# Kernel optimization log

Hardware: AMD Instinct MI355X
Metric: run time of the kernel (lower is better)

## Reference

```python
import jax, jax.numpy as jnp
import numpy as np

N, BOND, PHYS = 784, 4, 2
BS = 16384
STD = 1e-08


def setup_inputs() -> dict:
    key = jax.random.key(0)
    k1, k2 = jax.random.split(key)
    data = jax.random.randint(k1, (BS, N), 0, 2).astype(jnp.float32)
    bias = jnp.eye(BOND, dtype=jnp.float32)[:, :, None].repeat(PHYS, axis=2)  # (BOND,BOND,PHYS)
    tensors = STD * jax.random.normal(k2, (N, BOND, BOND, PHYS), dtype=jnp.float32) + bias
    return {"data": data, "tensors": tensors}


def reference(data, tensors):
    # data: (bs, n) in {0,1}; tensors: (n, D, D, P)
    bs, n = data.shape
    emb = jnp.stack([data, 1.0 - data], axis=2)  # (bs, n, P)
    # per-site transfer matrices for every sample: (n, bs, D, D)
    mats = jnp.einsum('nlri,bni->nblr', tensors, emb)
    left0 = mats[0][:, 0, :]  # (bs, D)  -- row 0 of site-0 matrix
    lx0 = jax.nn.log_softmax(tensors[0, 0, 0])  # (P,)

    def step(left, xs):
        t, m = xs  # t: (D, D, P), m: (bs, D, D)
        logits = left @ t[:, 0, :]              # (bs, P)
        lx = jax.nn.log_softmax(logits, axis=1)  # (bs, P)
        new_left = jnp.einsum('bl,blr->br', left, m)
        return new_left, lx

    _, lxs = jax.lax.scan(step, left0, (tensors[1:], mats[1:]))  # (n-1, bs, P)
    logx = jnp.concatenate(
        [jnp.broadcast_to(lx0, (1, bs, PHYS)), lxs], axis=0)  # (n, bs, P)
    logx = jnp.transpose(logx, (1, 0, 2))  # (bs, n, P)
    log_prob = logx[..., 0] * data + logx[..., 1] * (1.0 - data)
    return log_prob.sum(-1)  # (bs,)
```

## Files before the change

kernel.cpp:

```cpp
#include <hip/hip_runtime.h>

#define NSITES 784
#define BS_TOT 16384
#define KSEG 16
#define GSEG 49
#define NQUAD 12

typedef unsigned long long u64;

#define STEPV(sbit, TP, L0,L1,L2,L3, AN, AL) do {                                    \
    const float* t_ = (TP);                                                          \
    float p00 = fmaf(L0, t_[0],  fmaf(L1, t_[8],  fmaf(L2, t_[16], L3 * t_[24])));   \
    float p01 = fmaf(L0, t_[1],  fmaf(L1, t_[9],  fmaf(L2, t_[17], L3 * t_[25])));   \
    float p10 = fmaf(L0, t_[2],  fmaf(L1, t_[10], fmaf(L2, t_[18], L3 * t_[26])));   \
    float p11 = fmaf(L0, t_[3],  fmaf(L1, t_[11], fmaf(L2, t_[19], L3 * t_[27])));   \
    float p20 = fmaf(L0, t_[4],  fmaf(L1, t_[12], fmaf(L2, t_[20], L3 * t_[28])));   \
    float p21 = fmaf(L0, t_[5],  fmaf(L1, t_[13], fmaf(L2, t_[21], L3 * t_[29])));   \
    float p30 = fmaf(L0, t_[6],  fmaf(L1, t_[14], fmaf(L2, t_[22], L3 * t_[30])));   \
    float p31 = fmaf(L0, t_[7],  fmaf(L1, t_[15], fmaf(L2, t_[23], L3 * t_[31])));   \
    bool s_ = (sbit);                                                                \
    float mx_ = fmaxf(p00, p01);                                                     \
    float ch_ = s_ ? p00 : p01;                                                      \
    AN += (ch_ - mx_);                                                               \
    float ad_ = fabsf(p00 - p01);                                                    \
    AL += __builtin_amdgcn_logf(1.0f + __builtin_amdgcn_exp2f(-ad_ * 1.4426950408889634f)); \
    L0 = s_ ? p00 : p01;                                                             \
    L1 = s_ ? p10 : p11;                                                             \
    L2 = s_ ? p20 : p21;                                                             \
    L3 = s_ ? p30 : p31;                                                             \
} while (0)

#define STEP(sbit, TP) STEPV(sbit, TP, left0,left1,left2,left3, acc_nat, acc_l2)

#define MM_ROW(Q, Pr) do {                                                           \
    Q.x = fmaf(Pr.x, m0.x, fmaf(Pr.y, m1.x, fmaf(Pr.z, m2.x, Pr.w * m3.x)));         \
    Q.y = fmaf(Pr.x, m0.y, fmaf(Pr.y, m1.y, fmaf(Pr.z, m2.y, Pr.w * m3.y)));         \
    Q.z = fmaf(Pr.x, m0.z, fmaf(Pr.y, m1.z, fmaf(Pr.z, m2.z, Pr.w * m3.z)));         \
    Q.w = fmaf(Pr.x, m0.w, fmaf(Pr.y, m1.w, fmaf(Pr.z, m2.w, Pr.w * m3.w)));         \
} while (0)

#define MM4(P0,P1,P2,P3) do { float4 Q0,Q1,Q2,Q3; \
    MM_ROW(Q0,P0); MM_ROW(Q1,P1); MM_ROW(Q2,P2); MM_ROW(Q3,P3); \
    P0=Q0; P1=Q1; P2=Q2; P3=Q3; } while (0)

__global__ __launch_bounds__(256) void fused_pre_kernel(const float* __restrict__ tensors,
                                                        const float* __restrict__ data,
                                                        float* __restrict__ QQ,
                                                        u64* __restrict__ packed) {
    if (blockIdx.x < KSEG) {
        __shared__ float sPP[24][4][16];
        const int k = blockIdx.x;
        const int t = threadIdx.x;
        const int n0 = k * GSEG;

        if (t < 96) {
            const int j = t >> 2, c2 = t & 3;
            const float* t0 = tensors + (size_t)(n0 + 2 * j) * 32;
            const float* t1 = tensors + (size_t)(n0 + 2 * j + 1) * 32;
            const int p0 = (c2 & 1) ? 0 : 1;
            const int p1 = (c2 & 2) ? 0 : 1;
            float A[4][4], B[4][4];
            #pragma unroll
            for (int l = 0; l < 4; ++l)
                #pragma unroll
                for (int r = 0; r < 4; ++r) {
                    A[l][r] = t0[l * 8 + r * 2 + p0];
                    B[l][r] = t1[l * 8 + r * 2 + p1];
                }
            #pragma unroll
            for (int a = 0; a < 4; ++a)
                #pragma unroll
                for (int bb = 0; bb < 4; ++bb)
                    sPP[j][c2][a * 4 + bb] =
                        fmaf(A[a][0], B[0][bb], fmaf(A[a][1], B[1][bb],
                        fmaf(A[a][2], B[2][bb], A[a][3] * B[3][bb])));
        }
        __syncthreads();

        if (t < 192) {
            const int q = t >> 4, c = t & 15;
            const float* A = sPP[2 * q][c & 3];
            const float* B = sPP[2 * q + 1][(c >> 2) & 3];
            float* dst = QQ + ((size_t)(k * NQUAD + q) * 16 + c) * 16;
            #pragma unroll
            for (int a = 0; a < 4; ++a)
                #pragma unroll
                for (int bb = 0; bb < 4; ++bb)
                    dst[a * 4 + bb] =
                        fmaf(A[a * 4 + 0], B[0 * 4 + bb], fmaf(A[a * 4 + 1], B[1 * 4 + bb],
                        fmaf(A[a * 4 + 2], B[2 * 4 + bb], A[a * 4 + 3] * B[3 * 4 + bb])));
        }
    } else {
        int gid  = (blockIdx.x - KSEG) * 256 + threadIdx.x;
        int row  = gid >> 6;
        int lane = threadIdx.x & 63;
        const float* r = data + (size_t)row * NSITES;
        #pragma unroll
        for (int w = 0; w < 12; ++w) {
            u64 m = __ballot(r[w * 64 + lane] == 1.0f);
            if (lane == 0) packed[(size_t)w * BS_TOT + row] = m;
        }
        float v = (lane < 16) ? r[768 + lane] : 0.0f;
        u64 m = __ballot((lane < 16) && (v == 1.0f));
        if (lane == 0) packed[(size_t)12 * BS_TOT + row] = m;
    }
}

__device__ __forceinline__ u64 bit_window(const u64* __restrict__ packed, int n0, int b) {
    int a0 = n0 >> 6, s = n0 & 63;
    u64 w0 = packed[(size_t)a0 * BS_TOT + b];
    u64 w1 = packed[(size_t)(a0 + 1) * BS_TOT + b];
    return s ? ((w0 >> s) | (w1 << (64 - s))) : w0;
}

__global__ __launch_bounds__(256) void phase1q_kernel(const float* __restrict__ tensors,
                                                      const u64* __restrict__ packed,
                                                      const float* __restrict__ QQ,
                                                      float* __restrict__ Pbuf) {
    const int b = blockIdx.x * 256 + threadIdx.x;
    const int k = blockIdx.y;
    const int n0 = k * GSEG;

    __shared__ __align__(16) float lt[NQUAD * 16 * 20];
    {
        const float4* src = (const float4*)(QQ + (size_t)k * NQUAD * 16 * 16);
        float4* dst = (float4*)lt;
        for (int e = threadIdx.x; e < NQUAD * 16 * 4; e += 256) {
            int q = e >> 6, c = (e >> 2) & 15, j = e & 3;
            dst[q * 80 + c * 5 + j] = src[e];
        }
    }
    __syncthreads();

    u64 win = bit_window(packed, n0, b);
    const float4* ltf4 = (const float4*)lt;

    float4 P0, P1, P2, P3;
    {
        const int c0 = (int)(win & 15ull);
        const float4* mi = ltf4 + (c0 * 5);
        P0 = mi[0]; P1 = mi[1]; P2 = mi[2]; P3 = mi[3];
    }
    #pragma unroll
    for (int q = 1; q < NQUAD; ++q) {
        const int cq = (int)((win >> (4 * q)) & 15ull);
        const float4* mi = ltf4 + (q * 80 + cq * 5);
        float4 m0 = mi[0], m1 = mi[1], m2 = mi[2], m3 = mi[3];
        MM4(P0, P1, P2, P3);
    }
    {
        const float* t48 = tensors + (size_t)(n0 + 48) * 32;
        const bool s48 = ((win >> 48) & 1ull) != 0;
        float4 m0 = make_float4(s48 ? t48[0]  : t48[1],  s48 ? t48[2]  : t48[3],
                                s48 ? t48[4]  : t48[5],  s48 ? t48[6]  : t48[7]);
        float4 m1 = make_float4(s48 ? t48[8]  : t48[9],  s48 ? t48[10] : t48[11],
                                s48 ? t48[12] : t48[13], s48 ? t48[14] : t48[15]);
        float4 m2 = make_float4(s48 ? t48[16] : t48[17], s48 ? t48[18] : t48[19],
                                s48 ? t48[20] : t48[21], s48 ? t48[22] : t48[23]);
        float4 m3 = make_float4(s48 ? t48[24] : t48[25], s48 ? t48[26] : t48[27],
                                s48 ? t48[28] : t48[29], s48 ? t48[30] : t48[31]);
        MM4(P0, P1, P2, P3);
    }

    float4* pb = (float4*)(Pbuf + ((size_t)k * BS_TOT + b) * 16);
    pb[0] = P0; pb[1] = P1; pb[2] = P2; pb[3] = P3;
}

__global__ __launch_bounds__(256) void scan_kernel(const float* __restrict__ Pbuf,
                                                   float* __restrict__ prefix) {
    int b = blockIdx.x * 256 + threadIdx.x;
    float l0 = 1.0f, l1 = 0.0f, l2 = 0.0f, l3 = 0.0f;
    const float4* base = (const float4*)Pbuf + (size_t)b * 4;
    #pragma unroll
    for (int kc = 0; kc < 3; ++kc) {
        float4 R[5][4];
        #pragma unroll
        for (int j = 0; j < 5; ++j) {
            const float4* pb = base + (size_t)(kc * 5 + j) * BS_TOT * 4;
            R[j][0] = pb[0]; R[j][1] = pb[1]; R[j][2] = pb[2]; R[j][3] = pb[3];
        }
        #pragma unroll
        for (int j = 0; j < 5; ++j) {
            const int k = kc * 5 + j;
            prefix[((size_t)k * 4 + 0) * BS_TOT + b] = l0;
            prefix[((size_t)k * 4 + 1) * BS_TOT + b] = l1;
            prefix[((size_t)k * 4 + 2) * BS_TOT + b] = l2;
            prefix[((size_t)k * 4 + 3) * BS_TOT + b] = l3;
            float n0 = fmaf(l0, R[j][0].x, fmaf(l1, R[j][1].x, fmaf(l2, R[j][2].x, l3 * R[j][3].x)));
            float n1 = fmaf(l0, R[j][0].y, fmaf(l1, R[j][1].y, fmaf(l2, R[j][2].y, l3 * R[j][3].y)));
            float n2 = fmaf(l0, R[j][0].z, fmaf(l1, R[j][1].z, fmaf(l2, R[j][2].z, l3 * R[j][3].z)));
            float n3 = fmaf(l0, R[j][0].w, fmaf(l1, R[j][1].w, fmaf(l2, R[j][2].w, l3 * R[j][3].w)));
            l0 = n0; l1 = n1; l2 = n2; l3 = n3;
        }
    }
    prefix[((size_t)15 * 4 + 0) * BS_TOT + b] = l0;
    prefix[((size_t)15 * 4 + 1) * BS_TOT + b] = l1;
    prefix[((size_t)15 * 4 + 2) * BS_TOT + b] = l2;
    prefix[((size_t)15 * 4 + 3) * BS_TOT + b] = l3;
}

__global__ __launch_bounds__(256) void walk2_kernel(const float* __restrict__ tensors,
                                                    const u64* __restrict__ packed,
                                                    const float* __restrict__ prefix,
                                                    float* __restrict__ res) {
    const int k  = blockIdx.y;
    const int n0 = k * GSEG;
    const int b0 = blockIdx.x * 256 + threadIdx.x;
    const int b1 = b0 + BS_TOT / 2;
    const float* tb = tensors + (size_t)n0 * 32;

    u64 winA = bit_window(packed, n0, b0);
    u64 winB = bit_window(packed, n0, b1);

    float lA0 = prefix[((size_t)k * 4 + 0) * BS_TOT + b0];
    float lA1 = prefix[((size_t)k * 4 + 1) * BS_TOT + b0];
    float lA2 = prefix[((size_t)k * 4 + 2) * BS_TOT + b0];
    float lA3 = prefix[((size_t)k * 4 + 3) * BS_TOT + b0];
    float lB0 = prefix[((size_t)k * 4 + 0) * BS_TOT + b1];
    float lB1 = prefix[((size_t)k * 4 + 1) * BS_TOT + b1];
    float lB2 = prefix[((size_t)k * 4 + 2) * BS_TOT + b1];
    float lB3 = prefix[((size_t)k * 4 + 3) * BS_TOT + b1];
    float anA = 0.0f, alA = 0.0f, anB = 0.0f, alB = 0.0f;

    #pragma unroll 4
    for (int i = 0; i < GSEG; ++i) {
        const float* ts = tb + i * 32;
        STEPV(((winA >> i) & 1ull) != 0, ts, lA0,lA1,lA2,lA3, anA, alA);
        STEPV(((winB >> i) & 1ull) != 0, ts, lB0,lB1,lB2,lB3, anB, alB);
    }
    res[(size_t)k * BS_TOT + b0] = anA - 0.6931471805599453f * alA;
    res[(size_t)k * BS_TOT + b1] = anB - 0.6931471805599453f * alB;
}

__global__ __launch_bounds__(256) void reduce_kernel(const float* __restrict__ res,
                                                     float* __restrict__ out) {
    int b = blockIdx.x * 256 + threadIdx.x;
    float a = 0.0f;
    #pragma unroll
    for (int k = 0; k < KSEG; ++k) a += res[(size_t)k * BS_TOT + b];
    out[b] = a;
}

__global__ __launch_bounds__(64) void amps_chain_kernel(
    const float* __restrict__ data, const float* __restrict__ tensors,
    float* __restrict__ out)
{
    int b = blockIdx.x * blockDim.x + threadIdx.x;
    if (b >= BS_TOT) return;
    const float* row = data + (size_t)b * NSITES;
    float left0 = 1.0f, left1 = 0.0f, left2 = 0.0f, left3 = 0.0f;
    float acc_nat = 0.0f, acc_l2 = 0.0f;
    for (int n = 0; n < NSITES; ++n) {
        STEP(row[n] == 1.0f, tensors + (size_t)n * 32);
    }
    out[b] = acc_nat - 0.6931471805599453f * acc_l2;
}

extern "C" void kernel_launch(void* const* d_in, const int* in_sizes, int n_in,
                              void* d_out, int out_size, void* d_ws, size_t ws_size,
                              hipStream_t stream) {
    const float* data    = (const float*)d_in[0];
    const float* tensors = (const float*)d_in[1];
    float* out = (float*)d_out;

    const size_t packed_bytes = (size_t)13 * BS_TOT * 8;
    const size_t Pbuf_bytes   = (size_t)(KSEG - 1) * BS_TOT * 16 * 4;
    const size_t QQ_bytes     = (size_t)KSEG * NQUAD * 16 * 16 * 4;
    const size_t prefix_bytes = (size_t)KSEG * 4 * BS_TOT * 4;
    const size_t res_bytes    = (size_t)KSEG * BS_TOT * 4;
    const size_t need = packed_bytes + Pbuf_bytes + QQ_bytes + prefix_bytes + res_bytes;

    if (ws_size < need) {
        hipLaunchKernelGGL(amps_chain_kernel, dim3(BS_TOT / 64), dim3(64), 0, stream,
                           data, tensors, out);
        return;
    }

    char* wsb = (char*)d_ws;
    u64*   packed = (u64*)wsb;
    float* Pbuf   = (float*)(wsb + packed_bytes);
    float* QQ     = (float*)(wsb + packed_bytes + Pbuf_bytes);
    float* prefix = (float*)(wsb + packed_bytes + Pbuf_bytes + QQ_bytes);
    float* res    = (float*)(wsb + packed_bytes + Pbuf_bytes + QQ_bytes + prefix_bytes);

    hipLaunchKernelGGL(fused_pre_kernel, dim3(KSEG + (BS_TOT * 64) / 256), dim3(256), 0, stream,
                       tensors, data, QQ, packed);
    hipLaunchKernelGGL(phase1q_kernel,   dim3(BS_TOT / 256, KSEG - 1), dim3(256), 0, stream,
                       tensors, packed, QQ, Pbuf);
    hipLaunchKernelGGL(scan_kernel,      dim3(BS_TOT / 256), dim3(256), 0, stream,
                       Pbuf, prefix);
    hipLaunchKernelGGL(walk2_kernel,     dim3(BS_TOT / 2 / 256, KSEG), dim3(256), 0, stream,
                       tensors, packed, prefix, res);
    hipLaunchKernelGGL(reduce_kernel,    dim3(BS_TOT / 256), dim3(256), 0, stream, res, out);
}
```

Baseline: 65.43 us.

## Process four samples per thread in walk kernel with LDS-staged tensors

The segment walk kernel now handles four batch samples per thread instead of two, halving the grid. Each block first copies its segment's site tensors into shared memory and then reads them as float4 vectors, reused across the four independent chains. This aims to raise instruction-level parallelism and amortise tensor loads, at the cost of fewer blocks (one per CU), more registers, and a sync plus LDS copy up front.

```diff
diff --git a/kernel.cpp b/kernel.cpp
--- a/kernel.cpp
+++ b/kernel.cpp
@@ -8,29 +8,48 @@
 
 typedef unsigned long long u64;
 
-#define STEPV(sbit, TP, L0,L1,L2,L3, AN, AL) do {                                    \
+#define STEP_REGV(bitset, c0,c1,c2,c3,c4,c5,c6,c7, L0,L1,L2,L3, AN,AL) do { \
+  float p00 = fmaf(L0, c0.x, fmaf(L1, c2.x, fmaf(L2, c4.x, L3 * c6.x))); \
+  float p01 = fmaf(L0, c0.y, fmaf(L1, c2.y, fmaf(L2, c4.y, L3 * c6.y))); \
+  float p10 = fmaf(L0, c0.z, fmaf(L1, c2.z, fmaf(L2, c4.z, L3 * c6.z))); \
+  float p11 = fmaf(L0, c0.w, fmaf(L1, c2.w, fmaf(L2, c4.w, L3 * c6.w))); \
+  float p20 = fmaf(L0, c1.x, fmaf(L1, c3.x, fmaf(L2, c5.x, L3 * c7.x))); \
+  float p21 = fmaf(L0, c1.y, fmaf(L1, c3.y, fmaf(L2, c5.y, L3 * c7.y))); \
+  float p30 = fmaf(L0, c1.z, fmaf(L1, c3.z, fmaf(L2, c5.z, L3 * c7.z))); \
+  float p31 = fmaf(L0, c1.w, fmaf(L1, c3.w, fmaf(L2, c5.w, L3 * c7.w))); \
+  bool s_ = (bitset); \
+  float mx_ = fmaxf(p00, p01); \
+  float ch_ = s_ ? p00 : p01; \
+  AN += (ch_ - mx_); \
+  float ad_ = fabsf(p00 - p01); \
+  AL += __builtin_amdgcn_logf(1.0f + __builtin_amdgcn_exp2f(-ad_ * 1.4426950408889634f)); \
+  L0 = s_ ? p00 : p01; \
+  L1 = s_ ? p10 : p11; \
+  L2 = s_ ? p20 : p21; \
+  L3 = s_ ? p30 : p31; \
+} while (0)
+
+#define STEP(sbit, TP) do {                                                          \
     const float* t_ = (TP);                                                          \
-    float p00 = fmaf(L0, t_[0],  fmaf(L1, t_[8],  fmaf(L2, t_[16], L3 * t_[24])));   \
-    float p01 = fmaf(L0, t_[1],  fmaf(L1, t_[9],  fmaf(L2, t_[17], L3 * t_[25])));   \
-    float p10 = fmaf(L0, t_[2],  fmaf(L1, t_[10], fmaf(L2, t_[18], L3 * t_[26])));   \
-    float p11 = fmaf(L0, t_[3],  fmaf(L1, t_[11], fmaf(L2, t_[19], L3 * t_[27])));   \
-    float p20 = fmaf(L0, t_[4],  fmaf(L1, t_[12], fmaf(L2, t_[20], L3 * t_[28])));   \
-    float p21 = fmaf(L0, t_[5],  fmaf(L1, t_[13], fmaf(L2, t_[21], L3 * t_[29])));   \
-    float p30 = fmaf(L0, t_[6],  fmaf(L1, t_[14], fmaf(L2, t_[22], L3 * t_[30])));   \
-    float p31 = fmaf(L0, t_[7],  fmaf(L1, t_[15], fmaf(L2, t_[23], L3 * t_[31])));   \
+    float p00 = fmaf(left0, t_[0],  fmaf(left1, t_[8],  fmaf(left2, t_[16], left3 * t_[24]))); \
+    float p01 = fmaf(left0, t_[1],  fmaf(left1, t_[9],  fmaf(left2, t_[17], left3 * t_[25]))); \
+    float p10 = fmaf(left0, t_[2],  fmaf(left1, t_[10], fmaf(left2, t_[18], left3 * t_[26]))); \
+    float p11 = fmaf(left0, t_[3],  fmaf(left1, t_[11], fmaf(left2, t_[19], left3 * t_[27]))); \
+    float p20 = fmaf(left0, t_[4],  fmaf(left1, t_[12], fmaf(left2, t_[20], left3 * t_[28]))); \
+    float p21 = fmaf(left0, t_[5],  fmaf(left1, t_[13], fmaf(left2, t_[21], left3 * t_[29]))); \
+    float p30 = fmaf(left0, t_[6],  fmaf(left1, t_[14], fmaf(left2, t_[22], left3 * t_[30]))); \
+    float p31 = fmaf(left0, t_[7],  fmaf(left1, t_[15], fmaf(left2, t_[23], left3 * t_[31]))); \
     bool s_ = (sbit);                                                                \
     float mx_ = fmaxf(p00, p01);                                                     \
     float ch_ = s_ ? p00 : p01;                                                      \
-    AN += (ch_ - mx_);                                                               \
+    acc_nat += (ch_ - mx_);                                                          \
     float ad_ = fabsf(p00 - p01);                                                    \
-    AL += __builtin_amdgcn_logf(1.0f + __builtin_amdgcn_exp2f(-ad_ * 1.4426950408889634f)); \
-    L0 = s_ ? p00 : p01;                                                             \
-    L1 = s_ ? p10 : p11;                                                             \
-    L2 = s_ ? p20 : p21;                                                             \
-    L3 = s_ ? p30 : p31;                                                             \
+    acc_l2 += __builtin_amdgcn_logf(1.0f + __builtin_amdgcn_exp2f(-ad_ * 1.4426950408889634f)); \
+    left0 = s_ ? p00 : p01;                                                          \
+    left1 = s_ ? p10 : p11;                                                          \
+    left2 = s_ ? p20 : p21;                                                          \
+    left3 = s_ ? p30 : p31;                                                          \
 } while (0)
-
-#define STEP(sbit, TP) STEPV(sbit, TP, left0,left1,left2,left3, acc_nat, acc_l2)
 
 #define MM_ROW(Q, Pr) do {                                                           \
     Q.x = fmaf(Pr.x, m0.x, fmaf(Pr.y, m1.x, fmaf(Pr.z, m2.x, Pr.w * m3.x)));         \
@@ -199,37 +218,62 @@
     prefix[((size_t)15 * 4 + 3) * BS_TOT + b] = l3;
 }
 
-__global__ __launch_bounds__(256) void walk2_kernel(const float* __restrict__ tensors,
+__global__ __launch_bounds__(256) void walk4_kernel(const float* __restrict__ tensors,
                                                     const u64* __restrict__ packed,
                                                     const float* __restrict__ prefix,
                                                     float* __restrict__ res) {
     const int k  = blockIdx.y;
     const int n0 = k * GSEG;
-    const int b0 = blockIdx.x * 256 + threadIdx.x;
-    const int b1 = b0 + BS_TOT / 2;
-    const float* tb = tensors + (size_t)n0 * 32;
-
-    u64 winA = bit_window(packed, n0, b0);
-    u64 winB = bit_window(packed, n0, b1);
-
-    float lA0 = prefix[((size_t)k * 4 + 0) * BS_TOT + b0];
-    float lA1 = prefix[((size_t)k * 4 + 1) * BS_TOT + b0];
-    float lA2 = prefix[((size_t)k * 4 + 2) * BS_TOT + b0];
-    float lA3 = prefix[((size_t)k * 4 + 3) * BS_TOT + b0];
-    float lB0 = prefix[((size_t)k * 4 + 0) * BS_TOT + b1];
-    float lB1 = prefix[((size_t)k * 4 + 1) * BS_TOT + b1];
-    float lB2 = prefix[((size_t)k * 4 + 2) * BS_TOT + b1];
-    float lB3 = prefix[((size_t)k * 4 + 3) * BS_TOT + b1];
+
+    __shared__ __align__(16) float lt[GSEG * 32];
+    {
+        const float4* src = (const float4*)(tensors + (size_t)n0 * 32);
+        float4* dst = (float4*)lt;
+        for (int e = threadIdx.x; e < GSEG * 8; e += 256) dst[e] = src[e];
+    }
+    __syncthreads();
+
+    const int t  = threadIdx.x;
+    const int bA = blockIdx.x * 1024 + t;
+    const int bB = bA + 256;
+    const int bC = bA + 512;
+    const int bD = bA + 768;
+
+    u64 winA = bit_window(packed, n0, bA);
+    u64 winB = bit_window(packed, n0, bB);
+    u64 winC = bit_window(packed, n0, bC);
+    u64 winD = bit_window(packed, n0, bD);
+
+    const size_t pk = (size_t)k * 4 * BS_TOT;
+    float lA0 = prefix[pk + 0 * BS_TOT + bA], lA1 = prefix[pk + 1 * BS_TOT + bA];
+    float lA2 = prefix[pk + 2 * BS_TOT + bA], lA3 = prefix[pk + 3 * BS_TOT + bA];
+    float lB0 = prefix[pk + 0 * BS_TOT + bB], lB1 = prefix[pk + 1 * BS_TOT + bB];
+    float lB2 = prefix[pk + 2 * BS_TOT + bB], lB3 = prefix[pk + 3 * BS_TOT + bB];
+    float lC0 = prefix[pk + 0 * BS_TOT + bC], lC1 = prefix[pk + 1 * BS_TOT + bC];
+    float lC2 = prefix[pk + 2 * BS_TOT + bC], lC3 = prefix[pk + 3 * BS_TOT + bC];
+    float lD0 = prefix[pk + 0 * BS_TOT + bD], lD1 = prefix[pk + 1 * BS_TOT + bD];
+    float lD2 = prefix[pk + 2 * BS_TOT + bD], lD3 = prefix[pk + 3 * BS_TOT + bD];
     float anA = 0.0f, alA = 0.0f, anB = 0.0f, alB = 0.0f;
-
-    #pragma unroll 4
+    float anC = 0.0f, alC = 0.0f, anD = 0.0f, alD = 0.0f;
+
+    const float4* ltf4 = (const float4*)lt;
+    #pragma unroll 7
     for (int i = 0; i < GSEG; ++i) {
-        const float* ts = tb + i * 32;
-        STEPV(((winA >> i) & 1ull) != 0, ts, lA0,lA1,lA2,lA3, anA, alA);
-        STEPV(((winB >> i) & 1ull) != 0, ts, lB0,lB1,lB2,lB3, anB, alB);
-    }
-    res[(size_t)k * BS_TOT + b0] = anA - 0.6931471805599453f * alA;
-    res[(size_t)k * BS_TOT + b1] = anB - 0.6931471805599453f * alB;
+        float4 c0 = ltf4[i * 8 + 0], c1 = ltf4[i * 8 + 1];
+        float4 c2 = ltf4[i * 8 + 2], c3 = ltf4[i * 8 + 3];
+        float4 c4 = ltf4[i * 8 + 4], c5 = ltf4[i * 8 + 5];
+        float4 c6 = ltf4[i * 8 + 6], c7 = ltf4[i * 8 + 7];
+        STEP_REGV(((winA >> i) & 1ull) != 0, c0,c1,c2,c3,c4,c5,c6,c7, lA0,lA1,lA2,lA3, anA,alA);
+        STEP_REGV(((winB >> i) & 1ull) != 0, c0,c1,c2,c3,c4,c5,c6,c7, lB0,lB1,lB2,lB3, anB,alB);
+        STEP_REGV(((winC >> i) & 1ull) != 0, c0,c1,c2,c3,c4,c5,c6,c7, lC0,lC1,lC2,lC3, anC,alC);
+        STEP_REGV(((winD >> i) & 1ull) != 0, c0,c1,c2,c3,c4,c5,c6,c7, lD0,lD1,lD2,lD3, anD,alD);
+    }
+
+    const float LN2 = 0.6931471805599453f;
+    res[(size_t)k * BS_TOT + bA] = anA - LN2 * alA;
+    res[(size_t)k * BS_TOT + bB] = anB - LN2 * alB;
+    res[(size_t)k * BS_TOT + bC] = anC - LN2 * alC;
+    res[(size_t)k * BS_TOT + bD] = anD - LN2 * alD;
 }
 
 __global__ __launch_bounds__(256) void reduce_kernel(const float* __restrict__ res,
@@ -289,7 +333,7 @@
                        tensors, packed, QQ, Pbuf);
     hipLaunchKernelGGL(scan_kernel,      dim3(BS_TOT / 256), dim3(256), 0, stream,
                        Pbuf, prefix);
-    hipLaunchKernelGGL(walk2_kernel,     dim3(BS_TOT / 2 / 256, KSEG), dim3(256), 0, stream,
+    hipLaunchKernelGGL(walk4_kernel,     dim3(BS_TOT / 1024, KSEG), dim3(256), 0, stream,
                        tensors, packed, prefix, res);
     hipLaunchKernelGGL(reduce_kernel,    dim3(BS_TOT / 256), dim3(256), 0, stream, res, out);
 }
```

New measurement: 57.75 us. -11.7%, faster.
